# Kernel tuning notes

Measured on AMD Instinct MI355X. Metric: run time of the kernel, lower is better.

Reference implementation:

```python
import jax, jax.numpy as jnp
import numpy as np

WS = 8          # window_size
NH = 6          # num_heads
C = 192         # in_channels
HD = C // NH    # head_dim
N = WS * WS     # tokens per window


def _relative_position_index(ws):
    coords = np.stack(np.meshgrid(np.arange(ws), np.arange(ws), indexing='ij'), axis=-1).reshape(-1, 2)
    rel = coords[:, None, :] - coords[None, :, :] + (ws - 1)  # [N,N,2] in [0, 2ws-2]
    return (rel[..., 0] * (2 * ws - 1) + rel[..., 1]).astype(np.int32)  # [N,N]


def setup_inputs() -> dict:
    key = jax.random.key(0)
    ks = jax.random.split(key, 10)
    s = 0.02
    B, H, W = 8, 128, 128
    inp = {
        'x': jax.random.normal(ks[0], (B, C, H, W), dtype=jnp.float32),
        'qkv_w': jax.random.normal(ks[1], (3 * C, C), dtype=jnp.float32) * s,
        'qkv_b': jnp.zeros((3 * C,), dtype=jnp.float32),
        'proj_w': jax.random.normal(ks[2], (C, C), dtype=jnp.float32) * s,
        'proj_b': jnp.zeros((C,), dtype=jnp.float32),
        'mlp1_w': jax.random.normal(ks[3], (2 * C, C), dtype=jnp.float32) * s,
        'mlp1_b': jnp.zeros((2 * C,), dtype=jnp.float32),
        'mlp2_w': jax.random.normal(ks[4], (C, C), dtype=jnp.float32) * s,
        'mlp2_b': jnp.zeros((C,), dtype=jnp.float32),
        'bias_table': jax.random.normal(ks[5], ((2 * WS - 1) ** 2,), dtype=jnp.float32) * s,
        'rel_index': jnp.asarray(_relative_position_index(WS)),
    }
    return inp


def reference(x, qkv_w, qkv_b, proj_w, proj_b, mlp1_w, mlp1_b, mlp2_w, mlp2_b, bias_table, rel_index):
    B, _, H, W = x.shape
    nwh, nww = H // WS, W // WS
    # ---- window partition: [B,C,H,W] -> [B*nWin, N, C]
    xw = x.reshape(B, C, nwh, WS, nww, WS).transpose(0, 2, 4, 3, 5, 1).reshape(-1, N, C)
    # ---- qkv projection
    qkv = xw @ qkv_w.T + qkv_b  # [Bn, N, 3C]
    q, k, v = jnp.split(qkv, 3, axis=-1)
    split_heads = lambda t: t.reshape(-1, N, NH, HD).transpose(0, 2, 1, 3)  # [Bn,NH,N,HD]
    q, k, v = split_heads(q), split_heads(k), split_heads(v)
    # ---- learned relative-position bias (WindowScoreBias), broadcast over batch & heads
    bias = bias_table[rel_index]  # [N,N]
    scores = jnp.einsum('bhnd,bhmd->bhnm', q, k) * (1.0 / jnp.sqrt(jnp.float32(HD))) + bias
    attn = jax.nn.softmax(scores, axis=-1)
    out = jnp.einsum('bhnm,bhmd->bhnd', attn, v)  # [Bn,NH,N,HD]
    out = out.transpose(0, 2, 1, 3).reshape(-1, N, C)
    out = out @ proj_w.T + proj_b
    # ---- window merge back to BCHW
    out = out.reshape(B, nwh, nww, WS, WS, C).transpose(0, 5, 1, 3, 2, 4).reshape(B, C, H, W)
    x = x + out  # residual 1
    # ---- pointwise GLU MLP (1x1 convs as channel einsums)
    h = jnp.einsum('bchw,oc->bohw', x, mlp1_w) + mlp1_b[None, :, None, None]
    a, b = jnp.split(h, 2, axis=1)
    g = a * jax.nn.sigmoid(b)
    m = jnp.einsum('bchw,oc->bohw', g, mlp2_w) + mlp2_b[None, :, None, None]
    return x + m  # residual 2
```

## Files before the change

### kernel.cpp

```cpp
#include <hip/hip_runtime.h>


typedef short          s16x8 __attribute__((ext_vector_type(8)));
typedef unsigned short u16x4 __attribute__((ext_vector_type(4)));
typedef unsigned short u16x8 __attribute__((ext_vector_type(8)));
typedef float          f32x4 __attribute__((ext_vector_type(4)));

#define MFMA(A, B, C) __builtin_amdgcn_mfma_f32_16x16x32_bf16((A), (B), (C), 0, 0, 0)

__device__ __forceinline__ unsigned short f2b(float f) {
  unsigned x = __float_as_uint(f);
  x = (x + 0x7FFFu + ((x >> 16) & 1u)) >> 16;
  return (unsigned short)x;
}
__device__ __forceinline__ float b2f(unsigned short u) {
  return __uint_as_float(((unsigned)u) << 16);
}

__device__ __forceinline__ int swzQ(int t, int ch) {
  return t * 32 + ((((ch >> 3) ^ t) & 3) << 3) + (ch & 7);
}
__device__ __forceinline__ int swzP(int q, int k) {
  return q * 64 + ((((k >> 3) ^ q) & 7) << 3) + (k & 7);
}

#define XSTR   200
#define HSZ    6144
#define QSCALE 0.17677669529663687f

#define WOFF_QKV   0
#define WOFF_PROJ  110592
#define WOFF_MLP1  147456
#define WOFF_MLP2  221184
#define WOFF_BIASX_BYTES 516096
#define WOFF_YWIN_BYTES  532480

__global__ void prep_kernel(const float* __restrict__ qkv_w,
                            const float* __restrict__ proj_w,
                            const float* __restrict__ mlp1_w,
                            const float* __restrict__ mlp2_w,
                            const float* __restrict__ bias_table,
                            const int*   __restrict__ rel_index,
                            unsigned short* __restrict__ qkv_wb,
                            unsigned short* __restrict__ proj_wb,
                            unsigned short* __restrict__ mlp1_wb,
                            unsigned short* __restrict__ mlp2_wb,
                            float* __restrict__ biasx) {
  int j = blockIdx.x * 256 + threadIdx.x;
  if (j < 110592) {
    float v = qkv_w[j];
    if (j < 36864) v *= QSCALE;
    qkv_wb[j] = f2b(v);
  } else if (j < 147456) {
    proj_wb[j - 110592] = f2b(proj_w[j - 110592]);
  } else if (j < 221184) {
    mlp1_wb[j - 147456] = f2b(mlp1_w[j - 147456]);
  } else if (j < 258048) {
    mlp2_wb[j - 221184] = f2b(mlp2_w[j - 221184]);
  } else {
    int e = j - 258048;
    int l = e >> 6, v = e & 63;
    int tm = v >> 4, tn = (v >> 2) & 3, r = v & 3;
    int q = tn * 16 + (l & 15);
    int k = tm * 16 + (l >> 4) * 4 + r;
    biasx[e] = bias_table[rel_index[q * 64 + k]];
  }
}

__global__ __launch_bounds__(384, 3) void attn_kernel(
    const float* __restrict__ x,
    const unsigned short* __restrict__ qkv_wb, const float* __restrict__ qkv_b,
    const unsigned short* __restrict__ proj_wb, const float* __restrict__ proj_b,
    const float* __restrict__ biasx,
    unsigned short* __restrict__ y_win) {
  __shared__ __align__(16) unsigned short sm[6 * HSZ];

  const int tid  = threadIdx.x;
  const int lane = tid & 63;
  const int wv   = tid >> 6;
  const int l15  = lane & 15;
  const int lg   = lane >> 4;
  const int win  = ((blockIdx.x & 7) << 8) | (blockIdx.x >> 3);
  const int bb   = win >> 8;
  const int wh   = (win >> 4) & 15;
  const int wwi  = win & 15;

  unsigned short* xa = sm;
  const float* xwin = x + (size_t)bb * 192 * 16384 + (size_t)(wh * 8) * 128 + wwi * 8;

#pragma unroll
  for (int it = 0; it < 4; ++it) {
    int job = tid + 384 * it;
    int c = job >> 3, i = job & 7;
    const float* src = xwin + (size_t)c * 16384 + i * 128;
    f32x4 v0 = *(const f32x4*)(src);
    f32x4 v1 = *(const f32x4*)(src + 4);
    unsigned short* dst = &xa[(i * 8) * XSTR + c];
    dst[0 * XSTR] = f2b(v0[0]); dst[1 * XSTR] = f2b(v0[1]);
    dst[2 * XSTR] = f2b(v0[2]); dst[3 * XSTR] = f2b(v0[3]);
    dst[4 * XSTR] = f2b(v1[0]); dst[5 * XSTR] = f2b(v1[1]);
    dst[6 * XSTR] = f2b(v1[2]); dst[7 * XSTR] = f2b(v1[3]);
  }
  __syncthreads();

  unsigned short* hreg = sm + wv * HSZ;
  unsigned short* Qs  = hreg;
  unsigned short* Ks  = hreg + 2048;
  unsigned short* Vts = hreg + 4096;
  unsigned short* Ps  = hreg;
  unsigned short* AO  = hreg + 4096;

  f32x4 accq[4][2], acck[4][2], accv[4][2];
#pragma unroll
  for (int nt = 0; nt < 2; ++nt) {
    const int o = wv * 32 + nt * 16 + l15;
    const float bq = qkv_b[o] * QSCALE;
    const float bk = qkv_b[192 + o];
    const float bv = qkv_b[384 + o];
#pragma unroll
    for (int m = 0; m < 4; ++m) {
      accq[m][nt] = (f32x4){bq, bq, bq, bq};
      acck[m][nt] = (f32x4){bk, bk, bk, bk};
      accv[m][nt] = (f32x4){bv, bv, bv, bv};
    }
  }
#pragma unroll
  for (int ks = 0; ks < 6; ++ks) {
    const int k0 = ks * 32 + lg * 8;
    s16x8 af[4];
#pragma unroll
    for (int m = 0; m < 4; ++m)
      af[m] = *(const s16x8*)&xa[(m * 16 + l15) * XSTR + k0];
#pragma unroll
    for (int nt = 0; nt < 2; ++nt) {
      const int o = wv * 32 + nt * 16 + l15;
      s16x8 wq  = *(const s16x8*)&qkv_wb[(size_t)o * 192 + k0];
      s16x8 wk  = *(const s16x8*)&qkv_wb[(size_t)(192 + o) * 192 + k0];
      s16x8 wvv = *(const s16x8*)&qkv_wb[(size_t)(384 + o) * 192 + k0];
#pragma unroll
      for (int m = 0; m < 4; ++m) {
        accq[m][nt] = MFMA(af[m], wq , accq[m][nt]);
        acck[m][nt] = MFMA(af[m], wk , acck[m][nt]);
        accv[m][nt] = MFMA(af[m], wvv, accv[m][nt]);
      }
    }
  }
  u16x4 resv[4][2];
#pragma unroll
  for (int m = 0; m < 4; ++m)
#pragma unroll
    for (int nt = 0; nt < 2; ++nt)
#pragma unroll
      for (int r = 0; r < 4; ++r)
        resv[m][nt][r] = xa[(m * 16 + lg * 4 + r) * XSTR + wv * 32 + nt * 16 + l15];
  __syncthreads();

#pragma unroll
  for (int m = 0; m < 4; ++m) {
#pragma unroll
    for (int nt = 0; nt < 2; ++nt) {
      const int d = nt * 16 + l15;
#pragma unroll
      for (int r = 0; r < 4; ++r) {
        const int t = m * 16 + lg * 4 + r;
        Qs[swzQ(t, d)] = f2b(accq[m][nt][r]);
        Ks[swzQ(t, d)] = f2b(acck[m][nt][r]);
      }
      u16x4 pv;
      pv[0] = f2b(accv[m][nt][0]); pv[1] = f2b(accv[m][nt][1]);
      pv[2] = f2b(accv[m][nt][2]); pv[3] = f2b(accv[m][nt][3]);
      *(u16x4*)&Vts[swzP(d, m * 16 + lg * 4)] = pv;
    }
  }

  const float* bxp = biasx + lane * 64;
  s16x8 kf[4], qf[4];
#pragma unroll
  for (int tm = 0; tm < 4; ++tm)
    kf[tm] = *(const s16x8*)&Ks[swzQ(tm * 16 + l15, lg * 8)];
#pragma unroll
  for (int tn = 0; tn < 4; ++tn)
    qf[tn] = *(const s16x8*)&Qs[swzQ(tn * 16 + l15, lg * 8)];
  f32x4 sc[4][4];
#pragma unroll
  for (int tm = 0; tm < 4; ++tm)
#pragma unroll
    for (int tn = 0; tn < 4; ++tn) {
      f32x4 bfr = *(const f32x4*)&bxp[tm * 16 + tn * 4];
      sc[tm][tn] = MFMA(kf[tm], qf[tn], bfr);
    }
#pragma unroll
  for (int tn = 0; tn < 4; ++tn) {
    float mx = sc[0][tn][0];
#pragma unroll
    for (int tm = 0; tm < 4; ++tm)
#pragma unroll
      for (int r = 0; r < 4; ++r) mx = fmaxf(mx, sc[tm][tn][r]);
    mx = fmaxf(mx, __shfl_xor(mx, 16));
    mx = fmaxf(mx, __shfl_xor(mx, 32));
    float sum = 0.f;
#pragma unroll
    for (int tm = 0; tm < 4; ++tm)
#pragma unroll
      for (int r = 0; r < 4; ++r) {
        float e = __expf(sc[tm][tn][r] - mx);
        sc[tm][tn][r] = e;
        sum += e;
      }
    sum += __shfl_xor(sum, 16);
    sum += __shfl_xor(sum, 32);
    const float inv = 1.0f / sum;
#pragma unroll
    for (int tm = 0; tm < 4; ++tm)
#pragma unroll
      for (int r = 0; r < 4; ++r) sc[tm][tn][r] *= inv;
  }
#pragma unroll
  for (int tm = 0; tm < 4; ++tm)
#pragma unroll
    for (int tn = 0; tn < 4; ++tn) {
      u16x4 pv;
      pv[0] = f2b(sc[tm][tn][0]); pv[1] = f2b(sc[tm][tn][1]);
      pv[2] = f2b(sc[tm][tn][2]); pv[3] = f2b(sc[tm][tn][3]);
      *(u16x4*)&Ps[swzP(tn * 16 + l15, tm * 16 + lg * 4)] = pv;
    }

  f32x4 oacc[4][2];
#pragma unroll
  for (int m = 0; m < 4; ++m)
#pragma unroll
    for (int nt = 0; nt < 2; ++nt) oacc[m][nt] = (f32x4){0.f, 0.f, 0.f, 0.f};
#pragma unroll
  for (int ks = 0; ks < 2; ++ks) {
    s16x8 ap[4], bv2[2];
#pragma unroll
    for (int m = 0; m < 4; ++m)
      ap[m] = *(const s16x8*)&Ps[swzP(m * 16 + l15, ks * 32 + lg * 8)];
#pragma unroll
    for (int nt = 0; nt < 2; ++nt)
      bv2[nt] = *(const s16x8*)&Vts[swzP(nt * 16 + l15, ks * 32 + lg * 8)];
#pragma unroll
    for (int m = 0; m < 4; ++m)
#pragma unroll
      for (int nt = 0; nt < 2; ++nt)
        oacc[m][nt] = MFMA(ap[m], bv2[nt], oacc[m][nt]);
  }
#pragma unroll
  for (int m = 0; m < 4; ++m)
#pragma unroll
    for (int nt = 0; nt < 2; ++nt) {
      const int d = nt * 16 + l15;
#pragma unroll
      for (int r = 0; r < 4; ++r)
        AO[swzQ(m * 16 + lg * 4 + r, d)] = f2b(oacc[m][nt][r]);
    }
  __syncthreads();

  f32x4 pj[4][2];
#pragma unroll
  for (int nt = 0; nt < 2; ++nt) {
    const float bp = proj_b[wv * 32 + nt * 16 + l15];
#pragma unroll
    for (int m = 0; m < 4; ++m) pj[m][nt] = (f32x4){bp, bp, bp, bp};
  }
#pragma unroll
  for (int hh = 0; hh < 6; ++hh) {
    const unsigned short* aoh = sm + hh * HSZ + 4096;
    s16x8 aa[4];
#pragma unroll
    for (int m = 0; m < 4; ++m)
      aa[m] = *(const s16x8*)&aoh[swzQ(m * 16 + l15, lg * 8)];
#pragma unroll
    for (int nt = 0; nt < 2; ++nt) {
      s16x8 wp = *(const s16x8*)&proj_wb[(size_t)(wv * 32 + nt * 16 + l15) * 192 + hh * 32 + lg * 8];
#pragma unroll
      for (int m = 0; m < 4; ++m) pj[m][nt] = MFMA(aa[m], wp, pj[m][nt]);
    }
  }
  __syncthreads();

  unsigned short* ybuf = sm;
#pragma unroll
  for (int m = 0; m < 4; ++m)
#pragma unroll
    for (int nt = 0; nt < 2; ++nt) {
      const int o = wv * 32 + nt * 16 + l15;
#pragma unroll
      for (int r = 0; r < 4; ++r) {
        const int t = m * 16 + lg * 4 + r;
        ybuf[t * XSTR + o] = f2b(pj[m][nt][r] + b2f(resv[m][nt][r]));
      }
    }
  __syncthreads();
  unsigned short* ywp = y_win + (size_t)win * 12288;
#pragma unroll
  for (int it = 0; it < 4; ++it) {
    int job = tid + 384 * it;
    int t = job / 24;
    int seg = job - t * 24;
    *(u16x8*)&ywp[(size_t)job * 8] = *(const u16x8*)&ybuf[t * XSTR + seg * 8];
  }
}

__global__ __launch_bounds__(256) void mlp_kernel(
    const unsigned short* __restrict__ y_win,
    const unsigned short* __restrict__ w1b, const float* __restrict__ b1,
    const unsigned short* __restrict__ w2b, const float* __restrict__ b2,
    float* __restrict__ out) {
  __shared__ __align__(16) unsigned short sm2[2 * 64 * XSTR];
  unsigned short* yb = sm2;
  unsigned short* wk = sm2 + 64 * XSTR;

  const int tid  = threadIdx.x;
  const int lane = tid & 63;
  const int wv   = tid >> 6;
  const int l15  = lane & 15;
  const int lg   = lane >> 4;
  const int win  = ((blockIdx.x & 7) << 8) | (blockIdx.x >> 3);
  const int bb   = win >> 8;
  const int wh   = (win >> 4) & 15;
  const int wwi  = win & 15;

  const unsigned short* ywp = y_win + (size_t)win * 12288;
#pragma unroll
  for (int it = 0; it < 6; ++it) {
    int job = tid + 256 * it;
    int t = job / 24;
    int seg = job - t * 24;
    *(u16x8*)&yb[t * XSTR + seg * 8] = *(const u16x8*)&ywp[(size_t)job * 8];
  }
  __syncthreads();

  int ncol[6];
  f32x4 hacc[4][6];
#pragma unroll
  for (int i = 0; i < 6; ++i) {
    int ntile = (i < 3) ? (3 * wv + i) : (9 + 3 * wv + i);
    ncol[i] = ntile * 16 + l15;
    const float bb1 = b1[ncol[i]];
#pragma unroll
    for (int m = 0; m < 4; ++m) hacc[m][i] = (f32x4){bb1, bb1, bb1, bb1};
  }
#pragma unroll
  for (int ks = 0; ks < 6; ++ks) {
    const int k0 = ks * 32 + lg * 8;
    s16x8 af[4];
#pragma unroll
    for (int m = 0; m < 4; ++m)
      af[m] = *(const s16x8*)&yb[(m * 16 + l15) * XSTR + k0];
#pragma unroll
    for (int i = 0; i < 6; ++i) {
      s16x8 wf = *(const s16x8*)&w1b[(size_t)ncol[i] * 192 + k0];
#pragma unroll
      for (int m = 0; m < 4; ++m) hacc[m][i] = MFMA(af[m], wf, hacc[m][i]);
    }
  }
#pragma unroll
  for (int m = 0; m < 4; ++m)
#pragma unroll
    for (int i = 0; i < 3; ++i) {
#pragma unroll
      for (int r = 0; r < 4; ++r) {
        const float a = hacc[m][i][r];
        const float bg = hacc[m][i + 3][r];
        const float g = a * (1.0f / (1.0f + __expf(-bg)));
        wk[(m * 16 + lg * 4 + r) * XSTR + ncol[i]] = f2b(g);
      }
    }
  __syncthreads();

  int ocol[3];
  f32x4 macc[4][3];
#pragma unroll
  for (int i = 0; i < 3; ++i) {
    ocol[i] = (3 * wv + i) * 16 + l15;
    const float bb2 = b2[ocol[i]];
#pragma unroll
    for (int m = 0; m < 4; ++m) macc[m][i] = (f32x4){bb2, bb2, bb2, bb2};
  }
#pragma unroll
  for (int ks = 0; ks < 6; ++ks) {
    const int k0 = ks * 32 + lg * 8;
    s16x8 gf[4];
#pragma unroll
    for (int m = 0; m < 4; ++m)
      gf[m] = *(const s16x8*)&wk[(m * 16 + l15) * XSTR + k0];
#pragma unroll
    for (int i = 0; i < 3; ++i) {
      s16x8 wf = *(const s16x8*)&w2b[(size_t)ocol[i] * 192 + k0];
#pragma unroll
      for (int m = 0; m < 4; ++m) macc[m][i] = MFMA(gf[m], wf, macc[m][i]);
    }
  }
  __syncthreads();
#pragma unroll
  for (int m = 0; m < 4; ++m)
#pragma unroll
    for (int i = 0; i < 3; ++i)
#pragma unroll
      for (int r = 0; r < 4; ++r)
        wk[(m * 16 + lg * 4 + r) * XSTR + ocol[i]] = f2b(macc[m][i][r]);
  __syncthreads();

  float* obase = out + (size_t)bb * 192 * 16384 + (size_t)(wh * 8) * 128 + wwi * 8;
#pragma unroll
  for (int it = 0; it < 6; ++it) {
    int job = tid + 256 * it;
    int i = job / 192;
    int c = job - i * 192;
    float vals[8];
#pragma unroll
    for (int j = 0; j < 8; ++j) {
      const int t = i * 8 + j;
      vals[j] = b2f(yb[t * XSTR + c]) + b2f(wk[t * XSTR + c]);
    }
    float* dst = obase + (size_t)c * 16384 + i * 128;
    f32x4 o0 = {vals[0], vals[1], vals[2], vals[3]};
    f32x4 o1 = {vals[4], vals[5], vals[6], vals[7]};
    *(f32x4*)dst = o0;
    *(f32x4*)(dst + 4) = o1;
  }
}

extern "C" void kernel_launch(void* const* d_in, const int* in_sizes, int n_in,
                              void* d_out, int out_size, void* d_ws, size_t ws_size,
                              hipStream_t stream) {
  (void)in_sizes; (void)n_in; (void)out_size; (void)ws_size;
  const float* x          = (const float*)d_in[0];
  const float* qkv_w      = (const float*)d_in[1];
  const float* qkv_b      = (const float*)d_in[2];
  const float* proj_w     = (const float*)d_in[3];
  const float* proj_b     = (const float*)d_in[4];
  const float* mlp1_w     = (const float*)d_in[5];
  const float* mlp1_b     = (const float*)d_in[6];
  const float* mlp2_w     = (const float*)d_in[7];
  const float* mlp2_b     = (const float*)d_in[8];
  const float* bias_table = (const float*)d_in[9];
  const int*   rel_index  = (const int*)d_in[10];
  float* out = (float*)d_out;

  char* ws = (char*)d_ws;
  unsigned short* qkv_wb  = (unsigned short*)ws + WOFF_QKV;
  unsigned short* proj_wb = (unsigned short*)ws + WOFF_PROJ;
  unsigned short* mlp1_wb = (unsigned short*)ws + WOFF_MLP1;
  unsigned short* mlp2_wb = (unsigned short*)ws + WOFF_MLP2;
  float*          biasx   = (float*)(ws + WOFF_BIASX_BYTES);
  unsigned short* y_win   = (unsigned short*)(ws + WOFF_YWIN_BYTES);

  hipLaunchKernelGGL(prep_kernel, dim3(1024), dim3(256), 0, stream,
                     qkv_w, proj_w, mlp1_w, mlp2_w, bias_table, rel_index,
                     qkv_wb, proj_wb, mlp1_wb, mlp2_wb, biasx);
  hipLaunchKernelGGL(attn_kernel, dim3(2048), dim3(384), 0, stream,
                     x, qkv_wb, qkv_b, proj_wb, proj_b, biasx, y_win);
  hipLaunchKernelGGL(mlp_kernel, dim3(2048), dim3(256), 0, stream,
                     y_win, mlp1_wb, mlp1_b, mlp2_wb, mlp2_b, out);
}
```

Baseline: 282.3 us.

## Shrink per-head LDS scratch, split PV into two halves, rework input staging

Per-wave LDS scratch drops from 6144 to 4096 elements by reusing two 2048-element regions. P is written and consumed in two 32-key halves, and V^T is stored after softmax in the region that held K. The window input load now has each lane gather 8 channels at one spatial position and write them as one 16-byte LDS store, with a new swizzle for 32-wide rows. Lower LDS use per block may allow more resident blocks. The cost is that the global loads become strided scalar reads instead of float4 reads, and the P/V staging is serialised into two steps.

```diff
diff --git a/kernel.cpp b/kernel.cpp
--- a/kernel.cpp
+++ b/kernel.cpp
@@ -17,15 +17,15 @@
   return __uint_as_float(((unsigned)u) << 16);
 }
 
-__device__ __forceinline__ int swzQ(int t, int ch) {
-  return t * 32 + ((((ch >> 3) ^ t) & 3) << 3) + (ch & 7);
-}
-__device__ __forceinline__ int swzP(int q, int k) {
-  return q * 64 + ((((k >> 3) ^ q) & 7) << 3) + (k & 7);
+__device__ __forceinline__ int swz32(int t, int c) {
+  return t * 32 + ((((c >> 3) ^ (t >> 1)) & 3) << 3) + (c & 7);
+}
+__device__ __forceinline__ int swz64(int t, int c) {
+  return t * 64 + ((((c >> 3) ^ t) & 7) << 3) + (c & 7);
 }
 
 #define XSTR   200
-#define HSZ    6144
+#define HSZ    4096
 #define QSCALE 0.17677669529663687f
 
 #define WOFF_QKV   0
@@ -88,27 +88,23 @@
   unsigned short* xa = sm;
   const float* xwin = x + (size_t)bb * 192 * 16384 + (size_t)(wh * 8) * 128 + wwi * 8;
 
-#pragma unroll
-  for (int it = 0; it < 4; ++it) {
-    int job = tid + 384 * it;
-    int c = job >> 3, i = job & 7;
-    const float* src = xwin + (size_t)c * 16384 + i * 128;
-    f32x4 v0 = *(const f32x4*)(src);
-    f32x4 v1 = *(const f32x4*)(src + 4);
-    unsigned short* dst = &xa[(i * 8) * XSTR + c];
-    dst[0 * XSTR] = f2b(v0[0]); dst[1 * XSTR] = f2b(v0[1]);
-    dst[2 * XSTR] = f2b(v0[2]); dst[3 * XSTR] = f2b(v0[3]);
-    dst[4 * XSTR] = f2b(v1[0]); dst[5 * XSTR] = f2b(v1[1]);
-    dst[6 * XSTR] = f2b(v1[2]); dst[7 * XSTR] = f2b(v1[3]);
-  }
-  __syncthreads();
-
-  unsigned short* hreg = sm + wv * HSZ;
-  unsigned short* Qs  = hreg;
-  unsigned short* Ks  = hreg + 2048;
-  unsigned short* Vts = hreg + 4096;
-  unsigned short* Ps  = hreg;
-  unsigned short* AO  = hreg + 4096;
+  {
+    const int sp = ((lane >> 3) * 128) + (lane & 7);
+#pragma unroll
+    for (int it = 0; it < 4; ++it) {
+      const int chunk = it * 6 + wv;
+      const float* src = xwin + (size_t)(chunk * 8) * 16384 + sp;
+      u16x8 pk;
+#pragma unroll
+      for (int k = 0; k < 8; ++k) pk[k] = f2b(src[(size_t)k * 16384]);
+      *(u16x8*)&xa[lane * XSTR + chunk * 8] = pk;
+    }
+  }
+  __syncthreads();
+
+  unsigned short* hb = sm + wv * HSZ;
+  unsigned short* R0 = hb;
+  unsigned short* R1 = hb + 2048;
 
   f32x4 accq[4][2], acck[4][2], accv[4][2];
 #pragma unroll
@@ -156,31 +152,26 @@
   __syncthreads();
 
 #pragma unroll
-  for (int m = 0; m < 4; ++m) {
+  for (int m = 0; m < 4; ++m)
 #pragma unroll
     for (int nt = 0; nt < 2; ++nt) {
       const int d = nt * 16 + l15;
 #pragma unroll
       for (int r = 0; r < 4; ++r) {
         const int t = m * 16 + lg * 4 + r;
-        Qs[swzQ(t, d)] = f2b(accq[m][nt][r]);
-        Ks[swzQ(t, d)] = f2b(acck[m][nt][r]);
+        R0[swz32(t, d)] = f2b(accq[m][nt][r]);
+        R1[swz32(t, d)] = f2b(acck[m][nt][r]);
       }
-      u16x4 pv;
-      pv[0] = f2b(accv[m][nt][0]); pv[1] = f2b(accv[m][nt][1]);
-      pv[2] = f2b(accv[m][nt][2]); pv[3] = f2b(accv[m][nt][3]);
-      *(u16x4*)&Vts[swzP(d, m * 16 + lg * 4)] = pv;
-    }
-  }
+    }
 
   const float* bxp = biasx + lane * 64;
   s16x8 kf[4], qf[4];
 #pragma unroll
   for (int tm = 0; tm < 4; ++tm)
-    kf[tm] = *(const s16x8*)&Ks[swzQ(tm * 16 + l15, lg * 8)];
+    kf[tm] = *(const s16x8*)&R1[swz32(tm * 16 + l15, lg * 8)];
 #pragma unroll
   for (int tn = 0; tn < 4; ++tn)
-    qf[tn] = *(const s16x8*)&Qs[swzQ(tn * 16 + l15, lg * 8)];
+    qf[tn] = *(const s16x8*)&R0[swz32(tn * 16 + l15, lg * 8)];
   f32x4 sc[4][4];
 #pragma unroll
   for (int tm = 0; tm < 4; ++tm)
@@ -215,30 +206,41 @@
 #pragma unroll
       for (int r = 0; r < 4; ++r) sc[tm][tn][r] *= inv;
   }
-#pragma unroll
-  for (int tm = 0; tm < 4; ++tm)
+
+#pragma unroll
+  for (int m = 0; m < 4; ++m)
+#pragma unroll
+    for (int nt = 0; nt < 2; ++nt) {
+      const int d = nt * 16 + l15;
+      u16x4 pv;
+      pv[0] = f2b(accv[m][nt][0]); pv[1] = f2b(accv[m][nt][1]);
+      pv[2] = f2b(accv[m][nt][2]); pv[3] = f2b(accv[m][nt][3]);
+      *(u16x4*)&R1[swz64(d, m * 16 + lg * 4)] = pv;
+    }
+
+  f32x4 oacc[4][2];
+#pragma unroll
+  for (int m = 0; m < 4; ++m)
+#pragma unroll
+    for (int nt = 0; nt < 2; ++nt) oacc[m][nt] = (f32x4){0.f, 0.f, 0.f, 0.f};
+
+#pragma unroll
+  for (int tm = 0; tm < 2; ++tm)
 #pragma unroll
     for (int tn = 0; tn < 4; ++tn) {
       u16x4 pv;
       pv[0] = f2b(sc[tm][tn][0]); pv[1] = f2b(sc[tm][tn][1]);
       pv[2] = f2b(sc[tm][tn][2]); pv[3] = f2b(sc[tm][tn][3]);
-      *(u16x4*)&Ps[swzP(tn * 16 + l15, tm * 16 + lg * 4)] = pv;
-    }
-
-  f32x4 oacc[4][2];
-#pragma unroll
-  for (int m = 0; m < 4; ++m)
-#pragma unroll
-    for (int nt = 0; nt < 2; ++nt) oacc[m][nt] = (f32x4){0.f, 0.f, 0.f, 0.f};
-#pragma unroll
-  for (int ks = 0; ks < 2; ++ks) {
+      *(u16x4*)&R0[swz32(tn * 16 + l15, tm * 16 + lg * 4)] = pv;
+    }
+  {
     s16x8 ap[4], bv2[2];
 #pragma unroll
     for (int m = 0; m < 4; ++m)
-      ap[m] = *(const s16x8*)&Ps[swzP(m * 16 + l15, ks * 32 + lg * 8)];
+      ap[m] = *(const s16x8*)&R0[swz32(m * 16 + l15, lg * 8)];
 #pragma unroll
     for (int nt = 0; nt < 2; ++nt)
-      bv2[nt] = *(const s16x8*)&Vts[swzP(nt * 16 + l15, ks * 32 + lg * 8)];
+      bv2[nt] = *(const s16x8*)&R1[swz64(nt * 16 + l15, lg * 8)];
 #pragma unroll
     for (int m = 0; m < 4; ++m)
 #pragma unroll
@@ -246,13 +248,37 @@
         oacc[m][nt] = MFMA(ap[m], bv2[nt], oacc[m][nt]);
   }
 #pragma unroll
+  for (int tm = 2; tm < 4; ++tm)
+#pragma unroll
+    for (int tn = 0; tn < 4; ++tn) {
+      u16x4 pv;
+      pv[0] = f2b(sc[tm][tn][0]); pv[1] = f2b(sc[tm][tn][1]);
+      pv[2] = f2b(sc[tm][tn][2]); pv[3] = f2b(sc[tm][tn][3]);
+      *(u16x4*)&R0[swz32(tn * 16 + l15, (tm - 2) * 16 + lg * 4)] = pv;
+    }
+  {
+    s16x8 ap[4], bv2[2];
+#pragma unroll
+    for (int m = 0; m < 4; ++m)
+      ap[m] = *(const s16x8*)&R0[swz32(m * 16 + l15, lg * 8)];
+#pragma unroll
+    for (int nt = 0; nt < 2; ++nt)
+      bv2[nt] = *(const s16x8*)&R1[swz64(nt * 16 + l15, 32 + lg * 8)];
+#pragma unroll
+    for (int m = 0; m < 4; ++m)
+#pragma unroll
+      for (int nt = 0; nt < 2; ++nt)
+        oacc[m][nt] = MFMA(ap[m], bv2[nt], oacc[m][nt]);
+  }
+
+#pragma unroll
   for (int m = 0; m < 4; ++m)
 #pragma unroll
     for (int nt = 0; nt < 2; ++nt) {
       const int d = nt * 16 + l15;
 #pragma unroll
       for (int r = 0; r < 4; ++r)
-        AO[swzQ(m * 16 + lg * 4 + r, d)] = f2b(oacc[m][nt][r]);
+        R0[swz32(m * 16 + lg * 4 + r, d)] = f2b(oacc[m][nt][r]);
     }
   __syncthreads();
 
@@ -265,11 +291,11 @@
   }
 #pragma unroll
   for (int hh = 0; hh < 6; ++hh) {
-    const unsigned short* aoh = sm + hh * HSZ + 4096;
+    const unsigned short* aoh = sm + hh * HSZ;
     s16x8 aa[4];
 #pragma unroll
     for (int m = 0; m < 4; ++m)
-      aa[m] = *(const s16x8*)&aoh[swzQ(m * 16 + l15, lg * 8)];
+      aa[m] = *(const s16x8*)&aoh[swz32(m * 16 + l15, lg * 8)];
 #pragma unroll
     for (int nt = 0; nt < 2; ++nt) {
       s16x8 wp = *(const s16x8*)&proj_wb[(size_t)(wv * 32 + nt * 16 + l15) * 192 + hh * 32 + lg * 8];
```

Measured after the change: 356.1 us. 26.2% more time.

## Process two windows per attention block and cut register pressure in both kernels

Applied to the files above, without the earlier changes.

The attention kernel now handles two windows per 768-thread block, with one wave per head per window. It shrinks per-head LDS to two reusable 2048-element regions: Q/K are packed, V goes into the K region after the K fragments are loaded, and P is written in two halves. The residual add now reads x from shared memory instead of holding it in registers. Q/K accumulators are computed one nt tile at a time, and the MLP GLU stage computes the a/b pairs per column group to lower live accumulators, with launch bounds set to 4 blocks. The aim is higher occupancy and fewer launched blocks, at the risk of larger blocks limiting scheduling flexibility and extra reloads of the x fragments.

```diff
diff --git a/kernel.cpp b/kernel.cpp
--- a/kernel.cpp
+++ b/kernel.cpp
@@ -17,15 +17,15 @@
   return __uint_as_float(((unsigned)u) << 16);
 }
 
-__device__ __forceinline__ int swzQ(int t, int ch) {
-  return t * 32 + ((((ch >> 3) ^ t) & 3) << 3) + (ch & 7);
-}
-__device__ __forceinline__ int swzP(int q, int k) {
-  return q * 64 + ((((k >> 3) ^ q) & 7) << 3) + (k & 7);
+__device__ __forceinline__ int swz32(int t, int c) {
+  return t * 32 + ((((c >> 3) ^ (t >> 1)) & 3) << 3) + (c & 7);
+}
+__device__ __forceinline__ int swz64(int t, int c) {
+  return t * 64 + ((((c >> 3) ^ t) & 7) << 3) + (c & 7);
 }
 
 #define XSTR   200
-#define HSZ    6144
+#define WSLOT  37376
 #define QSCALE 0.17677669529663687f
 
 #define WOFF_QKV   0
@@ -67,13 +67,250 @@
   }
 }
 
-__global__ __launch_bounds__(384, 3) void attn_kernel(
+__global__ __launch_bounds__(768, 3) void attn_kernel(
     const float* __restrict__ x,
     const unsigned short* __restrict__ qkv_wb, const float* __restrict__ qkv_b,
     const unsigned short* __restrict__ proj_wb, const float* __restrict__ proj_b,
     const float* __restrict__ biasx,
     unsigned short* __restrict__ y_win) {
-  __shared__ __align__(16) unsigned short sm[6 * HSZ];
+  __shared__ __align__(16) unsigned short sm[2 * WSLOT];
+
+  const int tid  = threadIdx.x;
+  const int lane = tid & 63;
+  const int wv   = tid >> 6;
+  const int wid  = (wv >= 6) ? 1 : 0;
+  const int hd   = wv - wid * 6;
+  const int l15  = lane & 15;
+  const int lg   = lane >> 4;
+  const int pair = ((blockIdx.x & 7) << 7) | (blockIdx.x >> 3);
+  const int wins0 = pair * 2;
+
+  const float* xwb[2];
+#pragma unroll
+  for (int wi = 0; wi < 2; ++wi) {
+    const int w = wins0 + wi;
+    xwb[wi] = x + (size_t)(w >> 8) * 192 * 16384
+                + (size_t)(((w >> 4) & 15) * 8) * 128 + (w & 15) * 8;
+  }
+
+#pragma unroll
+  for (int it = 0; it < 4; ++it) {
+    int job = tid + 768 * it;
+    int wi = job / 1536;
+    int j = job - wi * 1536;
+    int c = j >> 3, i = j & 7;
+    const float* src = xwb[wi] + (size_t)c * 16384 + i * 128;
+    f32x4 v0 = *(const f32x4*)(src);
+    f32x4 v1 = *(const f32x4*)(src + 4);
+    unsigned short* dst = &sm[wi * WSLOT + (i * 8) * XSTR + c];
+    dst[0 * XSTR] = f2b(v0[0]); dst[1 * XSTR] = f2b(v0[1]);
+    dst[2 * XSTR] = f2b(v0[2]); dst[3 * XSTR] = f2b(v0[3]);
+    dst[4 * XSTR] = f2b(v1[0]); dst[5 * XSTR] = f2b(v1[1]);
+    dst[6 * XSTR] = f2b(v1[2]); dst[7 * XSTR] = f2b(v1[3]);
+  }
+  __syncthreads();
+
+  unsigned short* xa = sm + wid * WSLOT;
+  unsigned short* hb = xa + 12800 + hd * 4096;
+  unsigned short* R0 = hb;
+  unsigned short* R1 = hb + 2048;
+
+  f32x4 accv[4][2];
+#pragma unroll
+  for (int nt = 0; nt < 2; ++nt) {
+    const float bv = qkv_b[384 + hd * 32 + nt * 16 + l15];
+#pragma unroll
+    for (int m = 0; m < 4; ++m) accv[m][nt] = (f32x4){bv, bv, bv, bv};
+  }
+#pragma unroll
+  for (int nt = 0; nt < 2; ++nt) {
+    const int o = hd * 32 + nt * 16 + l15;
+    const float bq = qkv_b[o] * QSCALE;
+    const float bk = qkv_b[192 + o];
+    f32x4 accq[4], acck[4];
+#pragma unroll
+    for (int m = 0; m < 4; ++m) {
+      accq[m] = (f32x4){bq, bq, bq, bq};
+      acck[m] = (f32x4){bk, bk, bk, bk};
+    }
+#pragma unroll
+    for (int ks = 0; ks < 6; ++ks) {
+      const int k0 = ks * 32 + lg * 8;
+      s16x8 af[4];
+#pragma unroll
+      for (int m = 0; m < 4; ++m)
+        af[m] = *(const s16x8*)&xa[(m * 16 + l15) * XSTR + k0];
+      s16x8 wq  = *(const s16x8*)&qkv_wb[(size_t)o * 192 + k0];
+      s16x8 wk  = *(const s16x8*)&qkv_wb[(size_t)(192 + o) * 192 + k0];
+      s16x8 wvv = *(const s16x8*)&qkv_wb[(size_t)(384 + o) * 192 + k0];
+#pragma unroll
+      for (int m = 0; m < 4; ++m) {
+        accq[m] = MFMA(af[m], wq, accq[m]);
+        acck[m] = MFMA(af[m], wk, acck[m]);
+        accv[m][nt] = MFMA(af[m], wvv, accv[m][nt]);
+      }
+    }
+#pragma unroll
+    for (int m = 0; m < 4; ++m)
+#pragma unroll
+      for (int r = 0; r < 4; ++r) {
+        const int t = m * 16 + lg * 4 + r;
+        const int d = nt * 16 + l15;
+        R0[swz32(t, d)] = f2b(accq[m][r]);
+        R1[swz32(t, d)] = f2b(acck[m][r]);
+      }
+  }
+  u16x4 vreg[4][2];
+#pragma unroll
+  for (int m = 0; m < 4; ++m)
+#pragma unroll
+    for (int nt = 0; nt < 2; ++nt) {
+      vreg[m][nt][0] = f2b(accv[m][nt][0]); vreg[m][nt][1] = f2b(accv[m][nt][1]);
+      vreg[m][nt][2] = f2b(accv[m][nt][2]); vreg[m][nt][3] = f2b(accv[m][nt][3]);
+    }
+
+  const float* bxp = biasx + lane * 64;
+  s16x8 kf[4], qf[4];
+#pragma unroll
+  for (int tm = 0; tm < 4; ++tm)
+    kf[tm] = *(const s16x8*)&R1[swz32(tm * 16 + l15, lg * 8)];
+#pragma unroll
+  for (int tn = 0; tn < 4; ++tn)
+    qf[tn] = *(const s16x8*)&R0[swz32(tn * 16 + l15, lg * 8)];
+#pragma unroll
+  for (int m = 0; m < 4; ++m)
+#pragma unroll
+    for (int nt = 0; nt < 2; ++nt)
+      *(u16x4*)&R1[swz64(nt * 16 + l15, m * 16 + lg * 4)] = vreg[m][nt];
+
+  f32x4 sc[4][4];
+#pragma unroll
+  for (int tm = 0; tm < 4; ++tm)
+#pragma unroll
+    for (int tn = 0; tn < 4; ++tn) {
+      f32x4 bfr = *(const f32x4*)&bxp[tm * 16 + tn * 4];
+      sc[tm][tn] = MFMA(kf[tm], qf[tn], bfr);
+    }
+#pragma unroll
+  for (int tn = 0; tn < 4; ++tn) {
+    float mx = sc[0][tn][0];
+#pragma unroll
+    for (int tm = 0; tm < 4; ++tm)
+#pragma unroll
+      for (int r = 0; r < 4; ++r) mx = fmaxf(mx, sc[tm][tn][r]);
+    mx = fmaxf(mx, __shfl_xor(mx, 16));
+    mx = fmaxf(mx, __shfl_xor(mx, 32));
+    float sum = 0.f;
+#pragma unroll
+    for (int tm = 0; tm < 4; ++tm)
+#pragma unroll
+      for (int r = 0; r < 4; ++r) {
+        float e = __expf(sc[tm][tn][r] - mx);
+        sc[tm][tn][r] = e;
+        sum += e;
+      }
+    sum += __shfl_xor(sum, 16);
+    sum += __shfl_xor(sum, 32);
+    const float inv = 1.0f / sum;
+#pragma unroll
+    for (int tm = 0; tm < 4; ++tm)
+#pragma unroll
+      for (int r = 0; r < 4; ++r) sc[tm][tn][r] *= inv;
+  }
+
+  f32x4 oacc[4][2];
+#pragma unroll
+  for (int m = 0; m < 4; ++m)
+#pragma unroll
+    for (int nt = 0; nt < 2; ++nt) oacc[m][nt] = (f32x4){0.f, 0.f, 0.f, 0.f};
+#pragma unroll
+  for (int half = 0; half < 2; ++half) {
+#pragma unroll
+    for (int tm = 0; tm < 2; ++tm)
+#pragma unroll
+      for (int tn = 0; tn < 4; ++tn) {
+        u16x4 pv;
+        pv[0] = f2b(sc[half * 2 + tm][tn][0]); pv[1] = f2b(sc[half * 2 + tm][tn][1]);
+        pv[2] = f2b(sc[half * 2 + tm][tn][2]); pv[3] = f2b(sc[half * 2 + tm][tn][3]);
+        *(u16x4*)&R0[swz32(tn * 16 + l15, tm * 16 + lg * 4)] = pv;
+      }
+    s16x8 ap[4], bv2[2];
+#pragma unroll
+    for (int m = 0; m < 4; ++m)
+      ap[m] = *(const s16x8*)&R0[swz32(m * 16 + l15, lg * 8)];
+#pragma unroll
+    for (int nt = 0; nt < 2; ++nt)
+      bv2[nt] = *(const s16x8*)&R1[swz64(nt * 16 + l15, half * 32 + lg * 8)];
+#pragma unroll
+    for (int m = 0; m < 4; ++m)
+#pragma unroll
+      for (int nt = 0; nt < 2; ++nt)
+        oacc[m][nt] = MFMA(ap[m], bv2[nt], oacc[m][nt]);
+  }
+#pragma unroll
+  for (int m = 0; m < 4; ++m)
+#pragma unroll
+    for (int nt = 0; nt < 2; ++nt) {
+      const int d = nt * 16 + l15;
+#pragma unroll
+      for (int r = 0; r < 4; ++r)
+        R0[swz32(m * 16 + lg * 4 + r, d)] = f2b(oacc[m][nt][r]);
+    }
+  __syncthreads();
+
+  f32x4 pj[4][2];
+#pragma unroll
+  for (int nt = 0; nt < 2; ++nt) {
+    const float bp = proj_b[hd * 32 + nt * 16 + l15];
+#pragma unroll
+    for (int m = 0; m < 4; ++m) pj[m][nt] = (f32x4){bp, bp, bp, bp};
+  }
+#pragma unroll
+  for (int hh = 0; hh < 6; ++hh) {
+    const unsigned short* aoh = xa + 12800 + hh * 4096;
+    s16x8 aa[4];
+#pragma unroll
+    for (int m = 0; m < 4; ++m)
+      aa[m] = *(const s16x8*)&aoh[swz32(m * 16 + l15, lg * 8)];
+#pragma unroll
+    for (int nt = 0; nt < 2; ++nt) {
+      s16x8 wp = *(const s16x8*)&proj_wb[(size_t)(hd * 32 + nt * 16 + l15) * 192 + hh * 32 + lg * 8];
+#pragma unroll
+      for (int m = 0; m < 4; ++m) pj[m][nt] = MFMA(aa[m], wp, pj[m][nt]);
+    }
+  }
+#pragma unroll
+  for (int m = 0; m < 4; ++m)
+#pragma unroll
+    for (int nt = 0; nt < 2; ++nt) {
+      const int o = hd * 32 + nt * 16 + l15;
+#pragma unroll
+      for (int r = 0; r < 4; ++r) {
+        const int t = m * 16 + lg * 4 + r;
+        xa[t * XSTR + o] = f2b(pj[m][nt][r] + b2f(xa[t * XSTR + o]));
+      }
+    }
+  __syncthreads();
+#pragma unroll
+  for (int it = 0; it < 4; ++it) {
+    int job = tid + 768 * it;
+    int wi = job / 1536;
+    int j = job - wi * 1536;
+    int t = j / 24;
+    int seg = j - t * 24;
+    unsigned short* ywp = y_win + (size_t)(wins0 + wi) * 12288;
+    *(u16x8*)&ywp[(size_t)j * 8] = *(const u16x8*)&sm[wi * WSLOT + t * XSTR + seg * 8];
+  }
+}
+
+__global__ __launch_bounds__(256, 4) void mlp_kernel(
+    const unsigned short* __restrict__ y_win,
+    const unsigned short* __restrict__ w1b, const float* __restrict__ b1,
+    const unsigned short* __restrict__ w2b, const float* __restrict__ b2,
+    float* __restrict__ out) {
+  __shared__ __align__(16) unsigned short sm2[2 * 64 * XSTR];
+  unsigned short* yb = sm2;
+  unsigned short* wk = sm2 + 64 * XSTR;
 
   const int tid  = threadIdx.x;
   const int lane = tid & 63;
@@ -85,242 +322,6 @@
   const int wh   = (win >> 4) & 15;
   const int wwi  = win & 15;
 
-  unsigned short* xa = sm;
-  const float* xwin = x + (size_t)bb * 192 * 16384 + (size_t)(wh * 8) * 128 + wwi * 8;
-
-#pragma unroll
-  for (int it = 0; it < 4; ++it) {
-    int job = tid + 384 * it;
-    int c = job >> 3, i = job & 7;
-    const float* src = xwin + (size_t)c * 16384 + i * 128;
-    f32x4 v0 = *(const f32x4*)(src);
-    f32x4 v1 = *(const f32x4*)(src + 4);
-    unsigned short* dst = &xa[(i * 8) * XSTR + c];
-    dst[0 * XSTR] = f2b(v0[0]); dst[1 * XSTR] = f2b(v0[1]);
-    dst[2 * XSTR] = f2b(v0[2]); dst[3 * XSTR] = f2b(v0[3]);
-    dst[4 * XSTR] = f2b(v1[0]); dst[5 * XSTR] = f2b(v1[1]);
-    dst[6 * XSTR] = f2b(v1[2]); dst[7 * XSTR] = f2b(v1[3]);
-  }
-  __syncthreads();
-
-  unsigned short* hreg = sm + wv * HSZ;
-  unsigned short* Qs  = hreg;
-  unsigned short* Ks  = hreg + 2048;
-  unsigned short* Vts = hreg + 4096;
-  unsigned short* Ps  = hreg;
-  unsigned short* AO  = hreg + 4096;
-
-  f32x4 accq[4][2], acck[4][2], accv[4][2];
-#pragma unroll
-  for (int nt = 0; nt < 2; ++nt) {
-    const int o = wv * 32 + nt * 16 + l15;
-    const float bq = qkv_b[o] * QSCALE;
-    const float bk = qkv_b[192 + o];
-    const float bv = qkv_b[384 + o];
-#pragma unroll
-    for (int m = 0; m < 4; ++m) {
-      accq[m][nt] = (f32x4){bq, bq, bq, bq};
-      acck[m][nt] = (f32x4){bk, bk, bk, bk};
-      accv[m][nt] = (f32x4){bv, bv, bv, bv};
-    }
-  }
-#pragma unroll
-  for (int ks = 0; ks < 6; ++ks) {
-    const int k0 = ks * 32 + lg * 8;
-    s16x8 af[4];
-#pragma unroll
-    for (int m = 0; m < 4; ++m)
-      af[m] = *(const s16x8*)&xa[(m * 16 + l15) * XSTR + k0];
-#pragma unroll
-    for (int nt = 0; nt < 2; ++nt) {
-      const int o = wv * 32 + nt * 16 + l15;
-      s16x8 wq  = *(const s16x8*)&qkv_wb[(size_t)o * 192 + k0];
-      s16x8 wk  = *(const s16x8*)&qkv_wb[(size_t)(192 + o) * 192 + k0];
-      s16x8 wvv = *(const s16x8*)&qkv_wb[(size_t)(384 + o) * 192 + k0];
-#pragma unroll
-      for (int m = 0; m < 4; ++m) {
-        accq[m][nt] = MFMA(af[m], wq , accq[m][nt]);
-        acck[m][nt] = MFMA(af[m], wk , acck[m][nt]);
-        accv[m][nt] = MFMA(af[m], wvv, accv[m][nt]);
-      }
-    }
-  }
-  u16x4 resv[4][2];
-#pragma unroll
-  for (int m = 0; m < 4; ++m)
-#pragma unroll
-    for (int nt = 0; nt < 2; ++nt)
-#pragma unroll
-      for (int r = 0; r < 4; ++r)
-        resv[m][nt][r] = xa[(m * 16 + lg * 4 + r) * XSTR + wv * 32 + nt * 16 + l15];
-  __syncthreads();
-
-#pragma unroll
-  for (int m = 0; m < 4; ++m) {
-#pragma unroll
-    for (int nt = 0; nt < 2; ++nt) {
-      const int d = nt * 16 + l15;
-#pragma unroll
-      for (int r = 0; r < 4; ++r) {
-        const int t = m * 16 + lg * 4 + r;
-        Qs[swzQ(t, d)] = f2b(accq[m][nt][r]);
-        Ks[swzQ(t, d)] = f2b(acck[m][nt][r]);
-      }
-      u16x4 pv;
-      pv[0] = f2b(accv[m][nt][0]); pv[1] = f2b(accv[m][nt][1]);
-      pv[2] = f2b(accv[m][nt][2]); pv[3] = f2b(accv[m][nt][3]);
-      *(u16x4*)&Vts[swzP(d, m * 16 + lg * 4)] = pv;
-    }
-  }
-
-  const float* bxp = biasx + lane * 64;
-  s16x8 kf[4], qf[4];
-#pragma unroll
-  for (int tm = 0; tm < 4; ++tm)
-    kf[tm] = *(const s16x8*)&Ks[swzQ(tm * 16 + l15, lg * 8)];
-#pragma unroll
-  for (int tn = 0; tn < 4; ++tn)
-    qf[tn] = *(const s16x8*)&Qs[swzQ(tn * 16 + l15, lg * 8)];
-  f32x4 sc[4][4];
-#pragma unroll
-  for (int tm = 0; tm < 4; ++tm)
-#pragma unroll
-    for (int tn = 0; tn < 4; ++tn) {
-      f32x4 bfr = *(const f32x4*)&bxp[tm * 16 + tn * 4];
-      sc[tm][tn] = MFMA(kf[tm], qf[tn], bfr);
-    }
-#pragma unroll
-  for (int tn = 0; tn < 4; ++tn) {
-    float mx = sc[0][tn][0];
-#pragma unroll
-    for (int tm = 0; tm < 4; ++tm)
-#pragma unroll
-      for (int r = 0; r < 4; ++r) mx = fmaxf(mx, sc[tm][tn][r]);
-    mx = fmaxf(mx, __shfl_xor(mx, 16));
-    mx = fmaxf(mx, __shfl_xor(mx, 32));
-    float sum = 0.f;
-#pragma unroll
-    for (int tm = 0; tm < 4; ++tm)
-#pragma unroll
-      for (int r = 0; r < 4; ++r) {
-        float e = __expf(sc[tm][tn][r] - mx);
-        sc[tm][tn][r] = e;
-        sum += e;
-      }
-    sum += __shfl_xor(sum, 16);
-    sum += __shfl_xor(sum, 32);
-    const float inv = 1.0f / sum;
-#pragma unroll
-    for (int tm = 0; tm < 4; ++tm)
-#pragma unroll
-      for (int r = 0; r < 4; ++r) sc[tm][tn][r] *= inv;
-  }
-#pragma unroll
-  for (int tm = 0; tm < 4; ++tm)
-#pragma unroll
-    for (int tn = 0; tn < 4; ++tn) {
-      u16x4 pv;
-      pv[0] = f2b(sc[tm][tn][0]); pv[1] = f2b(sc[tm][tn][1]);
-      pv[2] = f2b(sc[tm][tn][2]); pv[3] = f2b(sc[tm][tn][3]);
-      *(u16x4*)&Ps[swzP(tn * 16 + l15, tm * 16 + lg * 4)] = pv;
-    }
-
-  f32x4 oacc[4][2];
-#pragma unroll
-  for (int m = 0; m < 4; ++m)
-#pragma unroll
-    for (int nt = 0; nt < 2; ++nt) oacc[m][nt] = (f32x4){0.f, 0.f, 0.f, 0.f};
-#pragma unroll
-  for (int ks = 0; ks < 2; ++ks) {
-    s16x8 ap[4], bv2[2];
-#pragma unroll
-    for (int m = 0; m < 4; ++m)
-      ap[m] = *(const s16x8*)&Ps[swzP(m * 16 + l15, ks * 32 + lg * 8)];
-#pragma unroll
-    for (int nt = 0; nt < 2; ++nt)
-      bv2[nt] = *(const s16x8*)&Vts[swzP(nt * 16 + l15, ks * 32 + lg * 8)];
-#pragma unroll
-    for (int m = 0; m < 4; ++m)
-#pragma unroll
-      for (int nt = 0; nt < 2; ++nt)
-        oacc[m][nt] = MFMA(ap[m], bv2[nt], oacc[m][nt]);
-  }
-#pragma unroll
-  for (int m = 0; m < 4; ++m)
-#pragma unroll
-    for (int nt = 0; nt < 2; ++nt) {
-      const int d = nt * 16 + l15;
-#pragma unroll
-      for (int r = 0; r < 4; ++r)
-        AO[swzQ(m * 16 + lg * 4 + r, d)] = f2b(oacc[m][nt][r]);
-    }
-  __syncthreads();
-
-  f32x4 pj[4][2];
-#pragma unroll
-  for (int nt = 0; nt < 2; ++nt) {
-    const float bp = proj_b[wv * 32 + nt * 16 + l15];
-#pragma unroll
-    for (int m = 0; m < 4; ++m) pj[m][nt] = (f32x4){bp, bp, bp, bp};
-  }
-#pragma unroll
-  for (int hh = 0; hh < 6; ++hh) {
-    const unsigned short* aoh = sm + hh * HSZ + 4096;
-    s16x8 aa[4];
-#pragma unroll
-    for (int m = 0; m < 4; ++m)
-      aa[m] = *(const s16x8*)&aoh[swzQ(m * 16 + l15, lg * 8)];
-#pragma unroll
-    for (int nt = 0; nt < 2; ++nt) {
-      s16x8 wp = *(const s16x8*)&proj_wb[(size_t)(wv * 32 + nt * 16 + l15) * 192 + hh * 32 + lg * 8];
-#pragma unroll
-      for (int m = 0; m < 4; ++m) pj[m][nt] = MFMA(aa[m], wp, pj[m][nt]);
-    }
-  }
-  __syncthreads();
-
-  unsigned short* ybuf = sm;
-#pragma unroll
-  for (int m = 0; m < 4; ++m)
-#pragma unroll
-    for (int nt = 0; nt < 2; ++nt) {
-      const int o = wv * 32 + nt * 16 + l15;
-#pragma unroll
-      for (int r = 0; r < 4; ++r) {
-        const int t = m * 16 + lg * 4 + r;
-        ybuf[t * XSTR + o] = f2b(pj[m][nt][r] + b2f(resv[m][nt][r]));
-      }
-    }
-  __syncthreads();
-  unsigned short* ywp = y_win + (size_t)win * 12288;
-#pragma unroll
-  for (int it = 0; it < 4; ++it) {
-    int job = tid + 384 * it;
-    int t = job / 24;
-    int seg = job - t * 24;
-    *(u16x8*)&ywp[(size_t)job * 8] = *(const u16x8*)&ybuf[t * XSTR + seg * 8];
-  }
-}
-
-__global__ __launch_bounds__(256) void mlp_kernel(
-    const unsigned short* __restrict__ y_win,
-    const unsigned short* __restrict__ w1b, const float* __restrict__ b1,
-    const unsigned short* __restrict__ w2b, const float* __restrict__ b2,
-    float* __restrict__ out) {
-  __shared__ __align__(16) unsigned short sm2[2 * 64 * XSTR];
-  unsigned short* yb = sm2;
-  unsigned short* wk = sm2 + 64 * XSTR;
-
-  const int tid  = threadIdx.x;
-  const int lane = tid & 63;
-  const int wv   = tid >> 6;
-  const int l15  = lane & 15;
-  const int lg   = lane >> 4;
-  const int win  = ((blockIdx.x & 7) << 8) | (blockIdx.x >> 3);
-  const int bb   = win >> 8;
-  const int wh   = (win >> 4) & 15;
-  const int wwi  = win & 15;
-
   const unsigned short* ywp = y_win + (size_t)win * 12288;
 #pragma unroll
   for (int it = 0; it < 6; ++it) {
@@ -331,42 +332,40 @@
   }
   __syncthreads();
 
-  int ncol[6];
-  f32x4 hacc[4][6];
-#pragma unroll
-  for (int i = 0; i < 6; ++i) {
-    int ntile = (i < 3) ? (3 * wv + i) : (9 + 3 * wv + i);
-    ncol[i] = ntile * 16 + l15;
-    const float bb1 = b1[ncol[i]];
-#pragma unroll
-    for (int m = 0; m < 4; ++m) hacc[m][i] = (f32x4){bb1, bb1, bb1, bb1};
-  }
-#pragma unroll
-  for (int ks = 0; ks < 6; ++ks) {
-    const int k0 = ks * 32 + lg * 8;
-    s16x8 af[4];
-#pragma unroll
-    for (int m = 0; m < 4; ++m)
-      af[m] = *(const s16x8*)&yb[(m * 16 + l15) * XSTR + k0];
-#pragma unroll
-    for (int i = 0; i < 6; ++i) {
-      s16x8 wf = *(const s16x8*)&w1b[(size_t)ncol[i] * 192 + k0];
-#pragma unroll
-      for (int m = 0; m < 4; ++m) hacc[m][i] = MFMA(af[m], wf, hacc[m][i]);
-    }
-  }
-#pragma unroll
-  for (int m = 0; m < 4; ++m)
-#pragma unroll
-    for (int i = 0; i < 3; ++i) {
+#pragma unroll
+  for (int i = 0; i < 3; ++i) {
+    const int na = (3 * wv + i) * 16 + l15;
+    const int nb = na + 192;
+    f32x4 aacc[4], bacc[4];
+    const float ba = b1[na], bbv = b1[nb];
+#pragma unroll
+    for (int m = 0; m < 4; ++m) {
+      aacc[m] = (f32x4){ba, ba, ba, ba};
+      bacc[m] = (f32x4){bbv, bbv, bbv, bbv};
+    }
+#pragma unroll
+    for (int ks = 0; ks < 6; ++ks) {
+      const int k0 = ks * 32 + lg * 8;
+      s16x8 af[4];
+#pragma unroll
+      for (int m = 0; m < 4; ++m)
+        af[m] = *(const s16x8*)&yb[(m * 16 + l15) * XSTR + k0];
+      s16x8 wa = *(const s16x8*)&w1b[(size_t)na * 192 + k0];
+      s16x8 wb = *(const s16x8*)&w1b[(size_t)nb * 192 + k0];
+#pragma unroll
+      for (int m = 0; m < 4; ++m) {
+        aacc[m] = MFMA(af[m], wa, aacc[m]);
+        bacc[m] = MFMA(af[m], wb, bacc[m]);
+      }
+    }
+#pragma unroll
+    for (int m = 0; m < 4; ++m)
 #pragma unroll
       for (int r = 0; r < 4; ++r) {
-        const float a = hacc[m][i][r];
-        const float bg = hacc[m][i + 3][r];
-        const float g = a * (1.0f / (1.0f + __expf(-bg)));
-        wk[(m * 16 + lg * 4 + r) * XSTR + ncol[i]] = f2b(g);
-      }
-    }
+        const float g = aacc[m][r] * (1.0f / (1.0f + __expf(-bacc[m][r])));
+        wk[(m * 16 + lg * 4 + r) * XSTR + na] = f2b(g);
+      }
+  }
   __syncthreads();
 
   int ocol[3];
@@ -450,7 +449,7 @@
   hipLaunchKernelGGL(prep_kernel, dim3(1024), dim3(256), 0, stream,
                      qkv_w, proj_w, mlp1_w, mlp2_w, bias_table, rel_index,
                      qkv_wb, proj_wb, mlp1_wb, mlp2_wb, biasx);
-  hipLaunchKernelGGL(attn_kernel, dim3(2048), dim3(384), 0, stream,
+  hipLaunchKernelGGL(attn_kernel, dim3(1024), dim3(768), 0, stream,
                      x, qkv_wb, qkv_b, proj_wb, proj_b, biasx, y_win);
   hipLaunchKernelGGL(mlp_kernel, dim3(2048), dim3(256), 0, stream,
                      y_win, mlp1_wb, mlp1_b, mlp2_wb, mlp2_b, out);
```

New measurement: 243.3 us. 13.8% less time.
